# Optimization experiments

Hardware: AMD Instinct MI355X
Metric: run time of the kernel (lower is better)

Reference implementation:

```python
import jax, jax.numpy as jnp
import numpy as np

TEMPERATURE = 0.1

def setup_inputs() -> dict:
    key = jax.random.key(0)
    ks = jax.random.split(key, 6)
    B, K, D, H, N = 256, 32, 128, 256, 16
    z = jax.random.normal(ks[0], (B, K, D), dtype=jnp.float32)
    # edge MLP params: Linear(2D->H), GELU, Linear(H->D)
    W1 = jax.random.normal(ks[1], (2 * D, H), dtype=jnp.float32) * (1.0 / np.sqrt(2 * D))
    b1 = jnp.zeros((H,), dtype=jnp.float32)
    W2 = jax.random.normal(ks[2], (H, D), dtype=jnp.float32) * (1.0 / np.sqrt(H))
    b2 = jnp.zeros((D,), dtype=jnp.float32)
    codebook = jax.random.normal(ks[3], (N, D), dtype=jnp.float32) * 0.02
    return {"z": z, "W1": W1, "b1": b1, "W2": W2, "b2": b2, "codebook": codebook}

def reference(z, W1, b1, W2, b2, codebook):
    # z: (B,K,D). Edge MLP on concat([z_i, z_j]) == split-weight GEMMs,
    # avoiding materializing the (B,K,K,2D) concat tensor.
    D = z.shape[-1]
    h_i = jnp.einsum('bkd,dh->bkh', z, W1[:D])   # contribution of z_i
    h_j = jnp.einsum('bkd,dh->bkh', z, W1[D:])   # contribution of z_j
    h = h_i[:, :, None, :] + h_j[:, None, :, :] + b1       # (B,K,K,H)
    h = jax.nn.gelu(h, approximate=False)                    # torch nn.GELU default = exact erf
    e_ij = jnp.einsum('bijh,hd->bijd', h, W2) + b2           # (B,K,K,D)
    logits = jnp.einsum('bijd,nd->bijn', e_ij, codebook) / TEMPERATURE  # (B,K,K,N)
    alpha_ij = jax.nn.softmax(logits, axis=-1)
    m_ij = jnp.einsum('bijn,nd->bijd', alpha_ij, codebook)   # (B,K,K,D)
    return (m_ij, alpha_ij, e_ij, logits)
```

## Files before the change

kernel.cpp:

```cpp
#include <hip/hip_runtime.h>
#include <hip/hip_bf16.h>
#include <math.h>

#define BB 256
#define KK 32
#define DD 128
#define HH 256
#define NN 16
#define O0 ((size_t)0)
#define O1 ((size_t)33554432)
#define O2 ((size_t)37748736)
#define O3 ((size_t)71303168)

typedef float f32x4 __attribute__((ext_vector_type(4)));
typedef short s16x8 __attribute__((ext_vector_type(8)));

static __device__ __forceinline__ short f2bf(float x) {
  __hip_bfloat16 h = __float2bfloat16(x);
  return *reinterpret_cast<short*>(&h);
}
static __device__ __forceinline__ float bf2f(short s) {
  __hip_bfloat16 h;
  *reinterpret_cast<short*>(&h) = s;
  return __bfloat162float(h);
}
static __device__ __forceinline__ unsigned cvt_pk_bf16(float a, float b) {
  unsigned r;
  asm volatile("v_cvt_pk_bf16_f32 %0, %1, %2" : "=v"(r) : "v"(a), "v"(b));
  return r;
}

static __device__ __forceinline__ float gelu_exact(float x) {
  float ax = fabsf(x) * 0.70710678118654752f;
  float t = __builtin_amdgcn_rcpf(fmaf(0.3275911f, ax, 1.0f));
  float p = fmaf(1.061405429f, t, -1.453152027f);
  p = fmaf(p, t, 1.421413741f);
  p = fmaf(p, t, -0.284496736f);
  p = fmaf(p, t, 0.254829592f);
  p *= t;
  float e = __expf(-ax * ax);
  float er = fmaf(-p, e, 1.0f);
  er = copysignf(er, x);
  return 0.5f * x * (1.0f + er);
}

__global__ __launch_bounds__(256) void prep_kernel(
    const float* __restrict__ z, const float* __restrict__ W1,
    const float* __restrict__ W2, const float* __restrict__ cb,
    const float* __restrict__ b2,
    short* __restrict__ zb, short* __restrict__ W1th, short* __restrict__ W1tl,
    short* __restrict__ Wh, short* __restrict__ Wl, short* __restrict__ cbT,
    short* __restrict__ Vh, short* __restrict__ Vl, float* __restrict__ b2cb) {
  const int idx = blockIdx.x * 256 + threadIdx.x;
  zb[idx] = f2bf(z[idx]);
  if (idx < 512 * 128) {
    int c = idx >> 7, k = idx & 127;
    float w = (c < 256) ? W1[(size_t)k * 256 + c]
                        : W1[(size_t)(128 + k) * 256 + (c - 256)];
    short h = f2bf(w);
    W1th[idx] = h;
    W1tl[idx] = f2bf(w - bf2f(h));
  }
  if (idx < 128 * 256) {
    int c = idx >> 8, k = idx & 255;
    float w = W2[(size_t)k * 128 + c];
    short h = f2bf(w);
    Wh[idx] = h;
    Wl[idx] = f2bf(w - bf2f(h));
  }
  if (idx < 128 * 32) {
    int c = idx >> 5, n = idx & 31;
    cbT[idx] = (n < 16) ? f2bf(cb[(size_t)n * 128 + c]) : (short)0;
  }
  if (idx < 16 * 256) {
    int n = idx >> 8, k = idx & 255;
    float s = 0.f;
#pragma unroll 4
    for (int c = 0; c < 128; ++c)
      s += W2[(size_t)k * 128 + c] * cb[(size_t)n * 128 + c];
    short h = f2bf(s);
    Vh[idx] = h;
    Vl[idx] = f2bf(s - bf2f(h));
  }
  if (idx < 16) {
    float s = 0.f;
    for (int c = 0; c < 128; ++c) s += b2[c] * cb[(size_t)idx * 128 + c];
    b2cb[idx] = s;
  }
}

__global__ __launch_bounds__(256) void hproj_mfma(
    const short* __restrict__ zb, const short* __restrict__ W1th,
    const short* __restrict__ W1tl, const float* __restrict__ b1,
    float* __restrict__ H) {
  const int tid = threadIdx.x;
  const int lane = tid & 63;
  const int wv = tid >> 6;
  const int l4 = lane >> 4, l15 = lane & 15;
  const int row0 = blockIdx.x * 32;
  const int col0 = blockIdx.y * 128 + wv * 32;

  f32x4 acc[2][2];
#pragma unroll
  for (int mt = 0; mt < 2; ++mt)
#pragma unroll
    for (int nt = 0; nt < 2; ++nt)
      acc[mt][nt] = (f32x4){0.f, 0.f, 0.f, 0.f};

#pragma unroll
  for (int ks = 0; ks < 4; ++ks) {
    const int kof = ks * 32 + l4 * 8;
    s16x8 a0 = *(const s16x8*)(zb + (size_t)(row0 + l15) * 128 + kof);
    s16x8 a1 = *(const s16x8*)(zb + (size_t)(row0 + 16 + l15) * 128 + kof);
    s16x8 bh0 = *(const s16x8*)(W1th + (size_t)(col0 + l15) * 128 + kof);
    s16x8 bh1 = *(const s16x8*)(W1th + (size_t)(col0 + 16 + l15) * 128 + kof);
    s16x8 bl0 = *(const s16x8*)(W1tl + (size_t)(col0 + l15) * 128 + kof);
    s16x8 bl1 = *(const s16x8*)(W1tl + (size_t)(col0 + 16 + l15) * 128 + kof);
    acc[0][0] = __builtin_amdgcn_mfma_f32_16x16x32_bf16(a0, bh0, acc[0][0], 0, 0, 0);
    acc[0][0] = __builtin_amdgcn_mfma_f32_16x16x32_bf16(a0, bl0, acc[0][0], 0, 0, 0);
    acc[0][1] = __builtin_amdgcn_mfma_f32_16x16x32_bf16(a0, bh1, acc[0][1], 0, 0, 0);
    acc[0][1] = __builtin_amdgcn_mfma_f32_16x16x32_bf16(a0, bl1, acc[0][1], 0, 0, 0);
    acc[1][0] = __builtin_amdgcn_mfma_f32_16x16x32_bf16(a1, bh0, acc[1][0], 0, 0, 0);
    acc[1][0] = __builtin_amdgcn_mfma_f32_16x16x32_bf16(a1, bl0, acc[1][0], 0, 0, 0);
    acc[1][1] = __builtin_amdgcn_mfma_f32_16x16x32_bf16(a1, bh1, acc[1][1], 0, 0, 0);
    acc[1][1] = __builtin_amdgcn_mfma_f32_16x16x32_bf16(a1, bl1, acc[1][1], 0, 0, 0);
  }

#pragma unroll
  for (int nt = 0; nt < 2; ++nt) {
    const int col = col0 + nt * 16 + l15;
    const float bias = (col0 < 256) ? b1[col] : 0.f;
#pragma unroll
    for (int mt = 0; mt < 2; ++mt)
#pragma unroll
      for (int r = 0; r < 4; ++r)
        H[(size_t)(row0 + mt * 16 + l4 * 4 + r) * 512 + col] =
            acc[mt][nt][r] + bias;
  }
}

__global__ __launch_bounds__(256, 3) void pair_kernel(
    const float* __restrict__ Hcat, const short* __restrict__ Wh,
    const short* __restrict__ Wl, const float* __restrict__ b2,
    const short* __restrict__ Vh, const short* __restrict__ Vl,
    const float* __restrict__ b2cb, const short* __restrict__ cbT,
    float* __restrict__ out) {
  __shared__ short sAh[32 * 256];
  __shared__ short sAl[32 * 256];
  __shared__ short sAlp[32 * 32];

  const int tid = threadIdx.x;
  const int blk = blockIdx.x;
  const int b = blk >> 5;

  ((unsigned*)sAlp)[tid] = 0u;
  ((unsigned*)sAlp)[tid + 256] = 0u;

  {
    const int k0 = (tid & 127) * 2;
    const int pb = (tid >> 7) * 16;
    const float2 hiv = *(const float2*)(Hcat + (size_t)blk * 512 + k0);
    const float hx = hiv.x;
    const float hy = hiv.y;
    const float* hjp = Hcat + ((size_t)b * KK + pb) * 512 + 256 + k0;
    unsigned* aH = (unsigned*)sAh;
    unsigned* aL = (unsigned*)sAl;
    const int cw = tid & 127;
#pragma unroll 4
    for (int p = 0; p < 16; ++p) {
      const int row = pb + p;
      float2 hj = *(const float2*)(hjp + (size_t)p * 512);
      float g0 = gelu_exact(hx + hj.x);
      float g1 = gelu_exact(hy + hj.y);
      unsigned h01 = cvt_pk_bf16(g0, g1);
      float h0f = __uint_as_float(h01 << 16);
      float h1f = __uint_as_float(h01 & 0xFFFF0000u);
      unsigned l01 = cvt_pk_bf16(g0 - h0f, g1 - h1f);
      const int wi = row * 128 + ((cw ^ ((row & 7) << 2)));
      aH[wi] = h01;
      aL[wi] = l01;
    }
  }
  __syncthreads();

  const int lane = tid & 63;
  const int wv = tid >> 6;
  const int nb = wv * 32;
  const int l4 = lane >> 4;
  const int l15 = lane & 15;
  const int mtL = wv >> 1;

  f32x4 acc[2][2];
#pragma unroll
  for (int mt = 0; mt < 2; ++mt)
#pragma unroll
    for (int nt = 0; nt < 2; ++nt)
      acc[mt][nt] = (f32x4){0.f, 0.f, 0.f, 0.f};
  f32x4 lacc = (f32x4){0.f, 0.f, 0.f, 0.f};

  const int sw = (l15 & 7) << 4;
  const char* pAh = (const char*)sAh;
  const char* pAl = (const char*)sAl;
  const size_t gB0 = (size_t)(nb + l15) * 256 + l4 * 8;
  const size_t gV0 = (size_t)l15 * 256 + l4 * 8;

#pragma unroll
  for (int ks = 0; ks < 8; ++ks) {
    const int cbyte = ks * 64 + l4 * 16;
    const int o0 = l15 * 512 + (cbyte ^ sw);
    const int o1 = (16 + l15) * 512 + (cbyte ^ sw);
    s16x8 ah0 = *(const s16x8*)(pAh + o0);
    s16x8 ah1 = *(const s16x8*)(pAh + o1);
    s16x8 al0 = *(const s16x8*)(pAl + o0);
    s16x8 al1 = *(const s16x8*)(pAl + o1);
    const size_t g0 = gB0 + ks * 32;
    const size_t g1 = g0 + 16 * 256;
    s16x8 bh0 = *(const s16x8*)(Wh + g0);
    s16x8 bh1 = *(const s16x8*)(Wh + g1);
    s16x8 bl0 = *(const s16x8*)(Wl + g0);
    s16x8 bl1 = *(const s16x8*)(Wl + g1);

    acc[0][0] = __builtin_amdgcn_mfma_f32_16x16x32_bf16(ah0, bh0, acc[0][0], 0, 0, 0);
    acc[0][0] = __builtin_amdgcn_mfma_f32_16x16x32_bf16(al0, bh0, acc[0][0], 0, 0, 0);
    acc[0][0] = __builtin_amdgcn_mfma_f32_16x16x32_bf16(ah0, bl0, acc[0][0], 0, 0, 0);
    acc[0][1] = __builtin_amdgcn_mfma_f32_16x16x32_bf16(ah0, bh1, acc[0][1], 0, 0, 0);
    acc[0][1] = __builtin_amdgcn_mfma_f32_16x16x32_bf16(al0, bh1, acc[0][1], 0, 0, 0);
    acc[0][1] = __builtin_amdgcn_mfma_f32_16x16x32_bf16(ah0, bl1, acc[0][1], 0, 0, 0);
    acc[1][0] = __builtin_amdgcn_mfma_f32_16x16x32_bf16(ah1, bh0, acc[1][0], 0, 0, 0);
    acc[1][0] = __builtin_amdgcn_mfma_f32_16x16x32_bf16(al1, bh0, acc[1][0], 0, 0, 0);
    acc[1][0] = __builtin_amdgcn_mfma_f32_16x16x32_bf16(ah1, bl0, acc[1][0], 0, 0, 0);
    acc[1][1] = __builtin_amdgcn_mfma_f32_16x16x32_bf16(ah1, bh1, acc[1][1], 0, 0, 0);
    acc[1][1] = __builtin_amdgcn_mfma_f32_16x16x32_bf16(al1, bh1, acc[1][1], 0, 0, 0);
    acc[1][1] = __builtin_amdgcn_mfma_f32_16x16x32_bf16(ah1, bl1, acc[1][1], 0, 0, 0);

    s16x8 vh = *(const s16x8*)(Vh + gV0 + ks * 32);
    s16x8 vl = *(const s16x8*)(Vl + gV0 + ks * 32);
    s16x8 aHm = mtL ? ah1 : ah0;
    s16x8 aLm = mtL ? al1 : al0;
    lacc = __builtin_amdgcn_mfma_f32_16x16x32_bf16(aHm, vh, lacc, 0, 0, 0);
    lacc = __builtin_amdgcn_mfma_f32_16x16x32_bf16(aLm, vh, lacc, 0, 0, 0);
    lacc = __builtin_amdgcn_mfma_f32_16x16x32_bf16(aHm, vl, lacc, 0, 0, 0);
  }

  {
    const float b2v0 = b2[nb + l15];
    const float b2v1 = b2[nb + 16 + l15];
    float* eg = out + O2 + (size_t)blk * (KK * DD);
#pragma unroll
    for (int mt = 0; mt < 2; ++mt) {
#pragma unroll
      for (int r = 0; r < 4; ++r) {
        const int row = mt * 16 + l4 * 4 + r;
        eg[row * 128 + nb + l15] = acc[mt][0][r] + b2v0;
        eg[row * 128 + nb + 16 + l15] = acc[mt][1][r] + b2v1;
      }
    }
  }

  {
    const float b2cbv = b2cb[l15];
    const bool own = ((l4 >> 1) == (wv & 1));
    float* lg_out = out + O3 + (size_t)blk * (KK * NN);
    float* ag_out = out + O1 + (size_t)blk * (KK * NN);
#pragma unroll
    for (int r = 0; r < 4; ++r) {
      const int row = mtL * 16 + l4 * 4 + r;
      float lg = (lacc[r] + b2cbv) * 10.0f;
      float mx = lg;
#pragma unroll
      for (int m = 1; m < 16; m <<= 1) mx = fmaxf(mx, __shfl_xor(mx, m));
      float p = __expf(lg - mx);
      float s = p;
#pragma unroll
      for (int m = 1; m < 16; m <<= 1) s += __shfl_xor(s, m);
      float a = p / s;
      if (own) {
        lg_out[row * 16 + l15] = lg;
        ag_out[row * 16 + l15] = a;
        sAlp[row * 32 + l15] = f2bf(a);
      }
    }
  }
  __syncthreads();

  {
    float* mg = out + O0 + (size_t)blk * (KK * DD);
#pragma unroll
    for (int rg = 0; rg < 2; ++rg) {
      s16x8 af = *(const s16x8*)(sAlp + (rg * 16 + l15) * 32 + l4 * 8);
#pragma unroll
      for (int nt = 0; nt < 2; ++nt) {
        const int c = nb + nt * 16 + l15;
        s16x8 bf = *(const s16x8*)(cbT + (size_t)c * 32 + l4 * 8);
        f32x4 mac = (f32x4){0.f, 0.f, 0.f, 0.f};
        mac = __builtin_amdgcn_mfma_f32_16x16x32_bf16(af, bf, mac, 0, 0, 0);
#pragma unroll
        for (int r = 0; r < 4; ++r)
          mg[(rg * 16 + l4 * 4 + r) * 128 + c] = mac[r];
      }
    }
  }
}

extern "C" void kernel_launch(void* const* d_in, const int* in_sizes, int n_in,
                              void* d_out, int out_size, void* d_ws, size_t ws_size,
                              hipStream_t stream) {
  const float* z  = (const float*)d_in[0];
  const float* W1 = (const float*)d_in[1];
  const float* b1 = (const float*)d_in[2];
  const float* W2 = (const float*)d_in[3];
  const float* b2 = (const float*)d_in[4];
  const float* cb = (const float*)d_in[5];
  float* out = (float*)d_out;

  float* Hcat = (float*)d_ws;
  short* zb   = (short*)(Hcat + (size_t)8192 * 512);
  short* W1th = zb + (size_t)1048576;
  short* W1tl = W1th + (size_t)65536;
  short* Wh   = W1tl + (size_t)65536;
  short* Wl   = Wh + (size_t)32768;
  short* cbT  = Wl + (size_t)32768;
  short* Vh   = cbT + (size_t)4096;
  short* Vl   = Vh + (size_t)4096;
  float* b2cb = (float*)(Vl + (size_t)4096);

  prep_kernel<<<4096, 256, 0, stream>>>(z, W1, W2, cb, b2, zb, W1th, W1tl, Wh,
                                        Wl, cbT, Vh, Vl, b2cb);
  hproj_mfma<<<dim3(256, 4), 256, 0, stream>>>(zb, W1th, W1tl, b1, Hcat);
  pair_kernel<<<BB * KK, 256, 0, stream>>>(Hcat, Wh, Wl, b2, Vh, Vl, b2cb, cbT, out);
}
```

Baseline: 243.9 us.

## Process two rows per block, overlapping GELU generation with MFMA of previous row

Each pair_kernel block now handles two (b,i) rows. The GELU/bf16-split tile for the second row is computed into a second LDS buffer while the first row's GEMM MFMAs run, and the first row's codebook mixing MFMAs are interleaved into the second row's GEMM loop. The h_j rows are loaded once into registers and reused for both rows. The logit MFMAs are now done by only two waves instead of duplicated across all four. The cost is double LDS, more registers and occupancy lowered from 3 to 2 blocks, with half as many blocks in the grid.

New measurement: 229.0 us. -6.1%, faster.

```diff
diff --git a/kernel.cpp b/kernel.cpp
--- a/kernel.cpp
+++ b/kernel.cpp
@@ -139,46 +139,69 @@
   }
 }
 
-__global__ __launch_bounds__(256, 3) void pair_kernel(
+#define MFMA16(d, a, bsrc) d = __builtin_amdgcn_mfma_f32_16x16x32_bf16(a, bsrc, d, 0, 0, 0)
+
+#define GSTEP12()                                                              \
+  MFMA16(acc[0][0], ah0, bh0); MFMA16(acc[0][0], al0, bh0);                    \
+  MFMA16(acc[0][0], ah0, bl0);                                                 \
+  MFMA16(acc[0][1], ah0, bh1); MFMA16(acc[0][1], al0, bh1);                    \
+  MFMA16(acc[0][1], ah0, bl1);                                                 \
+  MFMA16(acc[1][0], ah1, bh0); MFMA16(acc[1][0], al1, bh0);                    \
+  MFMA16(acc[1][0], ah1, bl0);                                                 \
+  MFMA16(acc[1][1], ah1, bh1); MFMA16(acc[1][1], al1, bh1);                    \
+  MFMA16(acc[1][1], ah1, bl1);
+
+__global__ __launch_bounds__(256, 2) void pair_kernel(
     const float* __restrict__ Hcat, const short* __restrict__ Wh,
     const short* __restrict__ Wl, const float* __restrict__ b2,
     const short* __restrict__ Vh, const short* __restrict__ Vl,
     const float* __restrict__ b2cb, const short* __restrict__ cbT,
     float* __restrict__ out) {
-  __shared__ short sAh[32 * 256];
-  __shared__ short sAl[32 * 256];
-  __shared__ short sAlp[32 * 32];
+  __shared__ short A0h[32 * 256];
+  __shared__ short A0l[32 * 256];
+  __shared__ short A1hb[32 * 256];
+  __shared__ short A1lb[32 * 256];
+  __shared__ short Alp[2][32 * 32];
 
   const int tid = threadIdx.x;
-  const int blk = blockIdx.x;
-  const int b = blk >> 5;
-
-  ((unsigned*)sAlp)[tid] = 0u;
-  ((unsigned*)sAlp)[tid + 256] = 0u;
-
-  {
-    const int k0 = (tid & 127) * 2;
-    const int pb = (tid >> 7) * 16;
-    const float2 hiv = *(const float2*)(Hcat + (size_t)blk * 512 + k0);
-    const float hx = hiv.x;
-    const float hy = hiv.y;
+  const int q = blockIdx.x;
+  const size_t blk0 = (size_t)q * 2, blk1 = blk0 + 1;
+  const int b = q >> 4;
+
+  {
+    unsigned* az = (unsigned*)&Alp[0][0];
+    az[tid] = 0u; az[tid + 256] = 0u; az[tid + 512] = 0u; az[tid + 768] = 0u;
+  }
+
+  const int k0 = (tid & 127) * 2;
+  const int pb = (tid >> 7) * 16;
+  const int cw = tid & 127;
+
+  float2 hj2[16];
+  const float2 h0v = *(const float2*)(Hcat + blk0 * 512 + k0);
+  const float2 h1v = *(const float2*)(Hcat + blk1 * 512 + k0);
+  {
     const float* hjp = Hcat + ((size_t)b * KK + pb) * 512 + 256 + k0;
-    unsigned* aH = (unsigned*)sAh;
-    unsigned* aL = (unsigned*)sAl;
-    const int cw = tid & 127;
-#pragma unroll 4
+#pragma unroll
+    for (int p = 0; p < 16; ++p)
+      hj2[p] = *(const float2*)(hjp + (size_t)p * 512);
+  }
+
+  {
+    unsigned* aH = (unsigned*)A0h;
+    unsigned* aL = (unsigned*)A0l;
+#pragma unroll
     for (int p = 0; p < 16; ++p) {
       const int row = pb + p;
-      float2 hj = *(const float2*)(hjp + (size_t)p * 512);
-      float g0 = gelu_exact(hx + hj.x);
-      float g1 = gelu_exact(hy + hj.y);
-      unsigned h01 = cvt_pk_bf16(g0, g1);
-      float h0f = __uint_as_float(h01 << 16);
-      float h1f = __uint_as_float(h01 & 0xFFFF0000u);
-      unsigned l01 = cvt_pk_bf16(g0 - h0f, g1 - h1f);
-      const int wi = row * 128 + ((cw ^ ((row & 7) << 2)));
-      aH[wi] = h01;
-      aL[wi] = l01;
+      float g0 = gelu_exact(h0v.x + hj2[p].x);
+      float g1 = gelu_exact(h0v.y + hj2[p].y);
+      unsigned hpk = cvt_pk_bf16(g0, g1);
+      float f0 = __uint_as_float(hpk << 16);
+      float f1 = __uint_as_float(hpk & 0xFFFF0000u);
+      unsigned lpk = cvt_pk_bf16(g0 - f0, g1 - f1);
+      const int wi = row * 128 + (cw ^ ((row & 7) << 2));
+      aH[wi] = hpk;
+      aL[wi] = lpk;
     }
   }
   __syncthreads();
@@ -188,83 +211,87 @@
   const int nb = wv * 32;
   const int l4 = lane >> 4;
   const int l15 = lane & 15;
-  const int mtL = wv >> 1;
+  const int sw = (l15 & 7) << 4;
+  const size_t gB0 = (size_t)(nb + l15) * 256 + l4 * 8;
+  const size_t gV0 = (size_t)l15 * 256 + l4 * 8;
+  const bool lw = (wv < 2);
 
   f32x4 acc[2][2];
+  f32x4 lacc;
+
 #pragma unroll
   for (int mt = 0; mt < 2; ++mt)
 #pragma unroll
     for (int nt = 0; nt < 2; ++nt)
       acc[mt][nt] = (f32x4){0.f, 0.f, 0.f, 0.f};
-  f32x4 lacc = (f32x4){0.f, 0.f, 0.f, 0.f};
-
-  const int sw = (l15 & 7) << 4;
-  const char* pAh = (const char*)sAh;
-  const char* pAl = (const char*)sAl;
-  const size_t gB0 = (size_t)(nb + l15) * 256 + l4 * 8;
-  const size_t gV0 = (size_t)l15 * 256 + l4 * 8;
-
-#pragma unroll
-  for (int ks = 0; ks < 8; ++ks) {
-    const int cbyte = ks * 64 + l4 * 16;
-    const int o0 = l15 * 512 + (cbyte ^ sw);
-    const int o1 = (16 + l15) * 512 + (cbyte ^ sw);
-    s16x8 ah0 = *(const s16x8*)(pAh + o0);
-    s16x8 ah1 = *(const s16x8*)(pAh + o1);
-    s16x8 al0 = *(const s16x8*)(pAl + o0);
-    s16x8 al1 = *(const s16x8*)(pAl + o1);
-    const size_t g0 = gB0 + ks * 32;
-    const size_t g1 = g0 + 16 * 256;
-    s16x8 bh0 = *(const s16x8*)(Wh + g0);
-    s16x8 bh1 = *(const s16x8*)(Wh + g1);
-    s16x8 bl0 = *(const s16x8*)(Wl + g0);
-    s16x8 bl1 = *(const s16x8*)(Wl + g1);
-
-    acc[0][0] = __builtin_amdgcn_mfma_f32_16x16x32_bf16(ah0, bh0, acc[0][0], 0, 0, 0);
-    acc[0][0] = __builtin_amdgcn_mfma_f32_16x16x32_bf16(al0, bh0, acc[0][0], 0, 0, 0);
-    acc[0][0] = __builtin_amdgcn_mfma_f32_16x16x32_bf16(ah0, bl0, acc[0][0], 0, 0, 0);
-    acc[0][1] = __builtin_amdgcn_mfma_f32_16x16x32_bf16(ah0, bh1, acc[0][1], 0, 0, 0);
-    acc[0][1] = __builtin_amdgcn_mfma_f32_16x16x32_bf16(al0, bh1, acc[0][1], 0, 0, 0);
-    acc[0][1] = __builtin_amdgcn_mfma_f32_16x16x32_bf16(ah0, bl1, acc[0][1], 0, 0, 0);
-    acc[1][0] = __builtin_amdgcn_mfma_f32_16x16x32_bf16(ah1, bh0, acc[1][0], 0, 0, 0);
-    acc[1][0] = __builtin_amdgcn_mfma_f32_16x16x32_bf16(al1, bh0, acc[1][0], 0, 0, 0);
-    acc[1][0] = __builtin_amdgcn_mfma_f32_16x16x32_bf16(ah1, bl0, acc[1][0], 0, 0, 0);
-    acc[1][1] = __builtin_amdgcn_mfma_f32_16x16x32_bf16(ah1, bh1, acc[1][1], 0, 0, 0);
-    acc[1][1] = __builtin_amdgcn_mfma_f32_16x16x32_bf16(al1, bh1, acc[1][1], 0, 0, 0);
-    acc[1][1] = __builtin_amdgcn_mfma_f32_16x16x32_bf16(ah1, bl1, acc[1][1], 0, 0, 0);
-
-    s16x8 vh = *(const s16x8*)(Vh + gV0 + ks * 32);
-    s16x8 vl = *(const s16x8*)(Vl + gV0 + ks * 32);
-    s16x8 aHm = mtL ? ah1 : ah0;
-    s16x8 aLm = mtL ? al1 : al0;
-    lacc = __builtin_amdgcn_mfma_f32_16x16x32_bf16(aHm, vh, lacc, 0, 0, 0);
-    lacc = __builtin_amdgcn_mfma_f32_16x16x32_bf16(aLm, vh, lacc, 0, 0, 0);
-    lacc = __builtin_amdgcn_mfma_f32_16x16x32_bf16(aHm, vl, lacc, 0, 0, 0);
-  }
-
-  {
-    const float b2v0 = b2[nb + l15];
-    const float b2v1 = b2[nb + 16 + l15];
-    float* eg = out + O2 + (size_t)blk * (KK * DD);
-#pragma unroll
-    for (int mt = 0; mt < 2; ++mt) {
+  lacc = (f32x4){0.f, 0.f, 0.f, 0.f};
+  {
+    const char* pAh = (const char*)A0h;
+    const char* pAl = (const char*)A0l;
+    unsigned* aH = (unsigned*)A1hb;
+    unsigned* aL = (unsigned*)A1lb;
+#pragma unroll
+    for (int ks = 0; ks < 8; ++ks) {
+      const int cbyte = ks * 64 + l4 * 16;
+      const int o0 = l15 * 512 + (cbyte ^ sw);
+      const int o1 = (16 + l15) * 512 + (cbyte ^ sw);
+      s16x8 ah0 = *(const s16x8*)(pAh + o0);
+      s16x8 ah1 = *(const s16x8*)(pAh + o1);
+      s16x8 al0 = *(const s16x8*)(pAl + o0);
+      s16x8 al1 = *(const s16x8*)(pAl + o1);
+      const size_t g0 = gB0 + ks * 32;
+      const size_t g1 = g0 + 16 * 256;
+      s16x8 bh0 = *(const s16x8*)(Wh + g0);
+      s16x8 bh1 = *(const s16x8*)(Wh + g1);
+      s16x8 bl0 = *(const s16x8*)(Wl + g0);
+      s16x8 bl1 = *(const s16x8*)(Wl + g1);
+      GSTEP12()
+      if (lw) {
+        s16x8 vh = *(const s16x8*)(Vh + gV0 + ks * 32);
+        s16x8 vl = *(const s16x8*)(Vl + gV0 + ks * 32);
+        s16x8 aF = (wv == 1) ? ah1 : ah0;
+        s16x8 aG = (wv == 1) ? al1 : al0;
+        MFMA16(lacc, aF, vh);
+        MFMA16(lacc, aG, vh);
+        MFMA16(lacc, aF, vl);
+      }
+#pragma unroll
+      for (int pp = 0; pp < 2; ++pp) {
+        const int p = ks * 2 + pp;
+        const int row = pb + p;
+        float g0f = gelu_exact(h1v.x + hj2[p].x);
+        float g1f = gelu_exact(h1v.y + hj2[p].y);
+        unsigned hpk = cvt_pk_bf16(g0f, g1f);
+        float f0 = __uint_as_float(hpk << 16);
+        float f1 = __uint_as_float(hpk & 0xFFFF0000u);
+        unsigned lpk = cvt_pk_bf16(g0f - f0, g1f - f1);
+        const int wi = row * 128 + (cw ^ ((row & 7) << 2));
+        aH[wi] = hpk;
+        aL[wi] = lpk;
+      }
+    }
+  }
+
+  const float b2v0 = b2[nb + l15];
+  const float b2v1 = b2[nb + 16 + l15];
+  {
+    float* eg = out + O2 + blk0 * (KK * DD);
+#pragma unroll
+    for (int mt = 0; mt < 2; ++mt)
 #pragma unroll
       for (int r = 0; r < 4; ++r) {
         const int row = mt * 16 + l4 * 4 + r;
         eg[row * 128 + nb + l15] = acc[mt][0][r] + b2v0;
         eg[row * 128 + nb + 16 + l15] = acc[mt][1][r] + b2v1;
       }
-    }
-  }
-
-  {
-    const float b2cbv = b2cb[l15];
-    const bool own = ((l4 >> 1) == (wv & 1));
-    float* lg_out = out + O3 + (size_t)blk * (KK * NN);
-    float* ag_out = out + O1 + (size_t)blk * (KK * NN);
+  }
+  const float b2cbv = b2cb[l15];
+  if (lw) {
+    float* lg_out = out + O3 + blk0 * (KK * NN);
+    float* ag_out = out + O1 + blk0 * (KK * NN);
 #pragma unroll
     for (int r = 0; r < 4; ++r) {
-      const int row = mtL * 16 + l4 * 4 + r;
+      const int row = wv * 16 + l4 * 4 + r;
       float lg = (lacc[r] + b2cbv) * 10.0f;
       float mx = lg;
 #pragma unroll
@@ -274,26 +301,109 @@
 #pragma unroll
       for (int m = 1; m < 16; m <<= 1) s += __shfl_xor(s, m);
       float a = p / s;
-      if (own) {
-        lg_out[row * 16 + l15] = lg;
-        ag_out[row * 16 + l15] = a;
-        sAlp[row * 32 + l15] = f2bf(a);
-      }
+      lg_out[row * 16 + l15] = lg;
+      ag_out[row * 16 + l15] = a;
+      Alp[0][row * 32 + l15] = f2bf(a);
     }
   }
   __syncthreads();
 
-  {
-    float* mg = out + O0 + (size_t)blk * (KK * DD);
+#pragma unroll
+  for (int mt = 0; mt < 2; ++mt)
+#pragma unroll
+    for (int nt = 0; nt < 2; ++nt)
+      acc[mt][nt] = (f32x4){0.f, 0.f, 0.f, 0.f};
+  lacc = (f32x4){0.f, 0.f, 0.f, 0.f};
+  {
+    const char* pAh = (const char*)A1hb;
+    const char* pAl = (const char*)A1lb;
+    const short* alp0 = &Alp[0][0];
+    float* mg0 = out + O0 + blk0 * (KK * DD);
+#pragma unroll
+    for (int ks = 0; ks < 8; ++ks) {
+      const int cbyte = ks * 64 + l4 * 16;
+      const int o0 = l15 * 512 + (cbyte ^ sw);
+      const int o1 = (16 + l15) * 512 + (cbyte ^ sw);
+      s16x8 ah0 = *(const s16x8*)(pAh + o0);
+      s16x8 ah1 = *(const s16x8*)(pAh + o1);
+      s16x8 al0 = *(const s16x8*)(pAl + o0);
+      s16x8 al1 = *(const s16x8*)(pAl + o1);
+      const size_t g0 = gB0 + ks * 32;
+      const size_t g1 = g0 + 16 * 256;
+      s16x8 bh0 = *(const s16x8*)(Wh + g0);
+      s16x8 bh1 = *(const s16x8*)(Wh + g1);
+      s16x8 bl0 = *(const s16x8*)(Wl + g0);
+      s16x8 bl1 = *(const s16x8*)(Wl + g1);
+      GSTEP12()
+      if (lw) {
+        s16x8 vh = *(const s16x8*)(Vh + gV0 + ks * 32);
+        s16x8 vl = *(const s16x8*)(Vl + gV0 + ks * 32);
+        s16x8 aF = (wv == 1) ? ah1 : ah0;
+        s16x8 aG = (wv == 1) ? al1 : al0;
+        MFMA16(lacc, aF, vh);
+        MFMA16(lacc, aG, vh);
+        MFMA16(lacc, aF, vl);
+      }
+      if ((ks & 1) == 0) {
+        const int rg = ks >> 2;
+        const int nt = (ks >> 1) & 1;
+        s16x8 af = *(const s16x8*)(alp0 + (rg * 16 + l15) * 32 + l4 * 8);
+        const int c = nb + nt * 16 + l15;
+        s16x8 bf = *(const s16x8*)(cbT + (size_t)c * 32 + l4 * 8);
+        f32x4 mac = (f32x4){0.f, 0.f, 0.f, 0.f};
+        MFMA16(mac, af, bf);
+#pragma unroll
+        for (int r = 0; r < 4; ++r)
+          mg0[(rg * 16 + l4 * 4 + r) * 128 + c] = mac[r];
+      }
+    }
+  }
+
+  {
+    float* eg = out + O2 + blk1 * (KK * DD);
+#pragma unroll
+    for (int mt = 0; mt < 2; ++mt)
+#pragma unroll
+      for (int r = 0; r < 4; ++r) {
+        const int row = mt * 16 + l4 * 4 + r;
+        eg[row * 128 + nb + l15] = acc[mt][0][r] + b2v0;
+        eg[row * 128 + nb + 16 + l15] = acc[mt][1][r] + b2v1;
+      }
+  }
+  if (lw) {
+    float* lg_out = out + O3 + blk1 * (KK * NN);
+    float* ag_out = out + O1 + blk1 * (KK * NN);
+#pragma unroll
+    for (int r = 0; r < 4; ++r) {
+      const int row = wv * 16 + l4 * 4 + r;
+      float lg = (lacc[r] + b2cbv) * 10.0f;
+      float mx = lg;
+#pragma unroll
+      for (int m = 1; m < 16; m <<= 1) mx = fmaxf(mx, __shfl_xor(mx, m));
+      float p = __expf(lg - mx);
+      float s = p;
+#pragma unroll
+      for (int m = 1; m < 16; m <<= 1) s += __shfl_xor(s, m);
+      float a = p / s;
+      lg_out[row * 16 + l15] = lg;
+      ag_out[row * 16 + l15] = a;
+      Alp[1][row * 32 + l15] = f2bf(a);
+    }
+  }
+  __syncthreads();
+
+  {
+    float* mg = out + O0 + blk1 * (KK * DD);
+    const short* alp1 = &Alp[1][0];
 #pragma unroll
     for (int rg = 0; rg < 2; ++rg) {
-      s16x8 af = *(const s16x8*)(sAlp + (rg * 16 + l15) * 32 + l4 * 8);
+      s16x8 af = *(const s16x8*)(alp1 + (rg * 16 + l15) * 32 + l4 * 8);
 #pragma unroll
       for (int nt = 0; nt < 2; ++nt) {
         const int c = nb + nt * 16 + l15;
         s16x8 bf = *(const s16x8*)(cbT + (size_t)c * 32 + l4 * 8);
         f32x4 mac = (f32x4){0.f, 0.f, 0.f, 0.f};
-        mac = __builtin_amdgcn_mfma_f32_16x16x32_bf16(af, bf, mac, 0, 0, 0);
+        MFMA16(mac, af, bf);
 #pragma unroll
         for (int r = 0; r < 4; ++r)
           mg[(rg * 16 + l4 * 4 + r) * 128 + c] = mac[r];
@@ -327,5 +437,6 @@
   prep_kernel<<<4096, 256, 0, stream>>>(z, W1, W2, cb, b2, zb, W1th, W1tl, Wh,
                                         Wl, cbT, Vh, Vl, b2cb);
   hproj_mfma<<<dim3(256, 4), 256, 0, stream>>>(zb, W1th, W1tl, b1, Hcat);
-  pair_kernel<<<BB * KK, 256, 0, stream>>>(Hcat, Wh, Wl, b2, Vh, Vl, b2cb, cbT, out);
-}
+  pair_kernel<<<BB * KK / 2, 256, 0, stream>>>(Hcat, Wh, Wl, b2, Vh, Vl, b2cb,
+                                               cbT, out);
+}
```

## Transpose e_ij MFMA operands for float4 stores, limit logit MFMAs to two waves

Applied to the files above, without the earlier changes.

Swaps the A/B operands of the e_ij MFMAs so each lane holds four consecutive output columns, which allows vectorized float4 stores of e_ij with float4 bias loads. The logits MFMA and softmax now run only in waves 0-1, removing redundant work in waves 2-3. It also remaps blockIdx so consecutive launched blocks are strided across batches, and raises the launch-bounds occupancy hint from 3 to 4. The remap changes cache locality for the Hcat reads, and the higher occupancy target may constrain registers.

Result: faster. 232.3 us (-4.8%).

```diff
diff --git a/kernel.cpp b/kernel.cpp
--- a/kernel.cpp
+++ b/kernel.cpp
@@ -139,7 +139,9 @@
   }
 }
 
-__global__ __launch_bounds__(256, 3) void pair_kernel(
+#define MFMA16(d, a, bsrc) d = __builtin_amdgcn_mfma_f32_16x16x32_bf16(a, bsrc, d, 0, 0, 0)
+
+__global__ __launch_bounds__(256, 4) void pair_kernel(
     const float* __restrict__ Hcat, const short* __restrict__ Wh,
     const short* __restrict__ Wl, const float* __restrict__ b2,
     const short* __restrict__ Vh, const short* __restrict__ Vl,
@@ -150,7 +152,8 @@
   __shared__ short sAlp[32 * 32];
 
   const int tid = threadIdx.x;
-  const int blk = blockIdx.x;
+  const int d = blockIdx.x;
+  const int blk = (d & 7) * 1024 + (d >> 3);
   const int b = blk >> 5;
 
   ((unsigned*)sAlp)[tid] = 0u;
@@ -188,14 +191,14 @@
   const int nb = wv * 32;
   const int l4 = lane >> 4;
   const int l15 = lane & 15;
-  const int mtL = wv >> 1;
-
-  f32x4 acc[2][2];
-#pragma unroll
-  for (int mt = 0; mt < 2; ++mt)
-#pragma unroll
-    for (int nt = 0; nt < 2; ++nt)
-      acc[mt][nt] = (f32x4){0.f, 0.f, 0.f, 0.f};
+  const bool lw = (wv < 2);
+
+  f32x4 eacc[2][2];
+#pragma unroll
+  for (int w = 0; w < 2; ++w)
+#pragma unroll
+    for (int a = 0; a < 2; ++a)
+      eacc[w][a] = (f32x4){0.f, 0.f, 0.f, 0.f};
   f32x4 lacc = (f32x4){0.f, 0.f, 0.f, 0.f};
 
   const int sw = (l15 & 7) << 4;
@@ -220,61 +223,59 @@
     s16x8 bl0 = *(const s16x8*)(Wl + g0);
     s16x8 bl1 = *(const s16x8*)(Wl + g1);
 
-    acc[0][0] = __builtin_amdgcn_mfma_f32_16x16x32_bf16(ah0, bh0, acc[0][0], 0, 0, 0);
-    acc[0][0] = __builtin_amdgcn_mfma_f32_16x16x32_bf16(al0, bh0, acc[0][0], 0, 0, 0);
-    acc[0][0] = __builtin_amdgcn_mfma_f32_16x16x32_bf16(ah0, bl0, acc[0][0], 0, 0, 0);
-    acc[0][1] = __builtin_amdgcn_mfma_f32_16x16x32_bf16(ah0, bh1, acc[0][1], 0, 0, 0);
-    acc[0][1] = __builtin_amdgcn_mfma_f32_16x16x32_bf16(al0, bh1, acc[0][1], 0, 0, 0);
-    acc[0][1] = __builtin_amdgcn_mfma_f32_16x16x32_bf16(ah0, bl1, acc[0][1], 0, 0, 0);
-    acc[1][0] = __builtin_amdgcn_mfma_f32_16x16x32_bf16(ah1, bh0, acc[1][0], 0, 0, 0);
-    acc[1][0] = __builtin_amdgcn_mfma_f32_16x16x32_bf16(al1, bh0, acc[1][0], 0, 0, 0);
-    acc[1][0] = __builtin_amdgcn_mfma_f32_16x16x32_bf16(ah1, bl0, acc[1][0], 0, 0, 0);
-    acc[1][1] = __builtin_amdgcn_mfma_f32_16x16x32_bf16(ah1, bh1, acc[1][1], 0, 0, 0);
-    acc[1][1] = __builtin_amdgcn_mfma_f32_16x16x32_bf16(al1, bh1, acc[1][1], 0, 0, 0);
-    acc[1][1] = __builtin_amdgcn_mfma_f32_16x16x32_bf16(ah1, bl1, acc[1][1], 0, 0, 0);
-
-    s16x8 vh = *(const s16x8*)(Vh + gV0 + ks * 32);
-    s16x8 vl = *(const s16x8*)(Vl + gV0 + ks * 32);
-    s16x8 aHm = mtL ? ah1 : ah0;
-    s16x8 aLm = mtL ? al1 : al0;
-    lacc = __builtin_amdgcn_mfma_f32_16x16x32_bf16(aHm, vh, lacc, 0, 0, 0);
-    lacc = __builtin_amdgcn_mfma_f32_16x16x32_bf16(aLm, vh, lacc, 0, 0, 0);
-    lacc = __builtin_amdgcn_mfma_f32_16x16x32_bf16(aHm, vl, lacc, 0, 0, 0);
+    MFMA16(eacc[0][0], bh0, ah0); MFMA16(eacc[0][0], bh0, al0);
+    MFMA16(eacc[0][0], bl0, ah0);
+    MFMA16(eacc[0][1], bh0, ah1); MFMA16(eacc[0][1], bh0, al1);
+    MFMA16(eacc[0][1], bl0, ah1);
+    MFMA16(eacc[1][0], bh1, ah0); MFMA16(eacc[1][0], bh1, al0);
+    MFMA16(eacc[1][0], bl1, ah0);
+    MFMA16(eacc[1][1], bh1, ah1); MFMA16(eacc[1][1], bh1, al1);
+    MFMA16(eacc[1][1], bl1, ah1);
+
+    if (lw) {
+      s16x8 vh = *(const s16x8*)(Vh + gV0 + ks * 32);
+      s16x8 vl = *(const s16x8*)(Vl + gV0 + ks * 32);
+      s16x8 aF = (wv == 1) ? ah1 : ah0;
+      s16x8 aG = (wv == 1) ? al1 : al0;
+      MFMA16(lacc, aF, vh);
+      MFMA16(lacc, aG, vh);
+      MFMA16(lacc, aF, vl);
+    }
   }
 
   {
-    const float b2v0 = b2[nb + l15];
-    const float b2v1 = b2[nb + 16 + l15];
+    const float4 b2q0 = *(const float4*)(b2 + nb + l4 * 4);
+    const float4 b2q1 = *(const float4*)(b2 + nb + 16 + l4 * 4);
     float* eg = out + O2 + (size_t)blk * (KK * DD);
 #pragma unroll
-    for (int mt = 0; mt < 2; ++mt) {
-#pragma unroll
-      for (int r = 0; r < 4; ++r) {
-        const int row = mt * 16 + l4 * 4 + r;
-        eg[row * 128 + nb + l15] = acc[mt][0][r] + b2v0;
-        eg[row * 128 + nb + 16 + l15] = acc[mt][1][r] + b2v1;
-      }
+    for (int a = 0; a < 2; ++a) {
+      const int row = a * 16 + l15;
+      float4 v0 = make_float4(eacc[0][a][0] + b2q0.x, eacc[0][a][1] + b2q0.y,
+                              eacc[0][a][2] + b2q0.z, eacc[0][a][3] + b2q0.w);
+      float4 v1 = make_float4(eacc[1][a][0] + b2q1.x, eacc[1][a][1] + b2q1.y,
+                              eacc[1][a][2] + b2q1.z, eacc[1][a][3] + b2q1.w);
+      *(float4*)(eg + row * 128 + nb + l4 * 4) = v0;
+      *(float4*)(eg + row * 128 + nb + 16 + l4 * 4) = v1;
     }
   }
 
   {
     const float b2cbv = b2cb[l15];
-    const bool own = ((l4 >> 1) == (wv & 1));
-    float* lg_out = out + O3 + (size_t)blk * (KK * NN);
-    float* ag_out = out + O1 + (size_t)blk * (KK * NN);
-#pragma unroll
-    for (int r = 0; r < 4; ++r) {
-      const int row = mtL * 16 + l4 * 4 + r;
-      float lg = (lacc[r] + b2cbv) * 10.0f;
-      float mx = lg;
-#pragma unroll
-      for (int m = 1; m < 16; m <<= 1) mx = fmaxf(mx, __shfl_xor(mx, m));
-      float p = __expf(lg - mx);
-      float s = p;
-#pragma unroll
-      for (int m = 1; m < 16; m <<= 1) s += __shfl_xor(s, m);
-      float a = p / s;
-      if (own) {
+    if (lw) {
+      float* lg_out = out + O3 + (size_t)blk * (KK * NN);
+      float* ag_out = out + O1 + (size_t)blk * (KK * NN);
+#pragma unroll
+      for (int r = 0; r < 4; ++r) {
+        const int row = wv * 16 + l4 * 4 + r;
+        float lg = (lacc[r] + b2cbv) * 10.0f;
+        float mx = lg;
+#pragma unroll
+        for (int m = 1; m < 16; m <<= 1) mx = fmaxf(mx, __shfl_xor(mx, m));
+        float p = __expf(lg - mx);
+        float s = p;
+#pragma unroll
+        for (int m = 1; m < 16; m <<= 1) s += __shfl_xor(s, m);
+        float a = p / s;
         lg_out[row * 16 + l15] = lg;
         ag_out[row * 16 + l15] = a;
         sAlp[row * 32 + l15] = f2bf(a);
@@ -293,7 +294,7 @@
         const int c = nb + nt * 16 + l15;
         s16x8 bf = *(const s16x8*)(cbT + (size_t)c * 32 + l4 * 8);
         f32x4 mac = (f32x4){0.f, 0.f, 0.f, 0.f};
-        mac = __builtin_amdgcn_mfma_f32_16x16x32_bf16(af, bf, mac, 0, 0, 0);
+        MFMA16(mac, af, bf);
 #pragma unroll
         for (int r = 0; r < 4; ++r)
           mg[(rg * 16 + l4 * 4 + r) * 128 + c] = mac[r];
@@ -327,5 +328,6 @@
   prep_kernel<<<4096, 256, 0, stream>>>(z, W1, W2, cb, b2, zb, W1th, W1tl, Wh,
                                         Wl, cbT, Vh, Vl, b2cb);
   hproj_mfma<<<dim3(256, 4), 256, 0, stream>>>(zb, W1th, W1tl, b1, Hcat);
-  pair_kernel<<<BB * KK, 256, 0, stream>>>(Hcat, Wh, Wl, b2, Vh, Vl, b2cb, cbT, out);
-}
+  pair_kernel<<<BB * KK, 256, 0, stream>>>(Hcat, Wh, Wl, b2, Vh, Vl, b2cb,
+                                           cbT, out);
+}
```
